# Performance work log

Measured on AMD Instinct MI355X. Metric: run time of the kernel, lower is better.

## Reference

```python
import jax, jax.numpy as jnp
import numpy as np

N = 100000
E = 1000000
HID = 64


def gcn_conv(x, W, b, edge_index, edge_w, num_nodes):
    # PyG GCNConv with edge_weight: add self-loops (weight 1), symmetric norm,
    # out[c] = sum_e norm_e * (x @ W)[row_e] aggregated at col_e, plus bias.
    xw = x @ W  # [N, hid]
    row = jnp.concatenate([edge_index[0], jnp.arange(num_nodes)])
    col = jnp.concatenate([edge_index[1], jnp.arange(num_nodes)])
    ew = jnp.concatenate([edge_w, jnp.ones((num_nodes,), x.dtype)])
    deg = jax.ops.segment_sum(ew, col, num_segments=num_nodes)
    dinv = jnp.where(deg > 0, jax.lax.rsqrt(deg), 0.0)
    norm = dinv[row] * ew * dinv[col]  # [E+N]
    msgs = norm[:, None] * xw[row]  # [E+N, hid]
    out = jax.ops.segment_sum(msgs, col, num_segments=num_nodes)
    return out + b


def setup_inputs() -> dict:
    key = jax.random.key(0)
    ks = jax.random.split(key, 12)
    user_x = jax.random.normal(ks[0], (N, 3), jnp.float32)
    movie_x = jax.random.normal(ks[1], (N, 18), jnp.float32)
    edge_index = jax.random.randint(ks[2], (2, E), 0, N, jnp.int64)
    edge_attr = jax.random.uniform(ks[3], (E,), jnp.float32)
    def lin(k, fan_in, fan_out):
        bound = 1.0 / np.sqrt(fan_in)
        k1, k2 = jax.random.split(k)
        W = jax.random.uniform(k1, (fan_in, fan_out), jnp.float32, -bound, bound)
        b = jax.random.uniform(k2, (fan_out,), jnp.float32, -bound, bound)
        return W, b
    W_user, b_user = lin(ks[4], 3, HID)
    W_movie, b_movie = lin(ks[5], 18, HID)
    W1, b1 = lin(ks[6], 2 * HID, 128)
    W2, b2 = lin(ks[7], 128, 1)
    return {"user_x": user_x, "movie_x": movie_x, "edge_index": edge_index,
            "edge_attr": edge_attr, "W_user": W_user, "b_user": b_user,
            "W_movie": W_movie, "b_movie": b_movie, "W1": W1, "b1": b1,
            "W2": W2, "b2": b2}


def reference(user_x, movie_x, edge_index, edge_attr, W_user, b_user,
              W_movie, b_movie, W1, b1, W2, b2):
    user_out = gcn_conv(user_x, W_user, b_user, edge_index, edge_attr, N)
    movie_out = gcn_conv(movie_x, W_movie, b_movie, edge_index, edge_attr, N)
    h = jnp.concatenate([user_out, movie_out], axis=-1)  # [N, 128]
    h = jax.nn.relu(h @ W1 + b1)
    rating_pred = h @ W2 + b2  # [N, 1]
    return rating_pred
```

## Files before the change

### kernel.cpp

```cpp
#include <hip/hip_runtime.h>

#define NN 100000
#define NE 1000000
#define BSH 7
#define BCOLS 128
#define NBUCK 782
#define SBLK 256
#define CAP 2048

__global__ __launch_bounds__(128) void fuse_kernel(const float* __restrict__ Wu,
                                                   const float* __restrict__ bu,
                                                   const float* __restrict__ Wm,
                                                   const float* __restrict__ bm,
                                                   const float* __restrict__ W1,
                                                   const float* __restrict__ b1,
                                                   const float* __restrict__ W2,
                                                   float* __restrict__ Mt,
                                                   int* __restrict__ cnt) {
    const int j = threadIdx.x;
    for (int i = j; i < NBUCK; i += 128) cnt[i] = 0;

    float w1c[128];
#pragma unroll
    for (int k = 0; k < 128; k++) w1c[k] = W1[k * 128 + j];

    float* row = Mt + j * 24;
#pragma unroll
    for (int m = 0; m < 3; m++) {
        float acc = 0.f;
#pragma unroll
        for (int k = 0; k < 64; k++) acc = fmaf(Wu[m * 64 + k], w1c[k], acc);
        row[m] = acc;
    }
#pragma unroll
    for (int m = 0; m < 18; m++) {
        float acc = 0.f;
#pragma unroll
        for (int k = 0; k < 64; k++) acc = fmaf(Wm[m * 64 + k], w1c[64 + k], acc);
        row[3 + m] = acc;
    }
    float bp = b1[j];
#pragma unroll
    for (int k = 0; k < 64; k++) {
        bp = fmaf(bu[k], w1c[k], bp);
        bp = fmaf(bm[k], w1c[64 + k], bp);
    }
    row[21] = bp;
    row[22] = W2[j];
    row[23] = 0.f;
}

__global__ __launch_bounds__(256) void bcnt_kernel(const int* __restrict__ col,
                                                   int* __restrict__ cnt) {
    __shared__ int h[NBUCK];
    for (int i = threadIdx.x; i < NBUCK; i += 256) h[i] = 0;
    __syncthreads();
    for (int e = blockIdx.x * 256 + threadIdx.x; e < NE; e += SBLK * 256)
        atomicAdd(&h[col[e] >> BSH], 1);
    __syncthreads();
    for (int i = threadIdx.x; i < NBUCK; i += 256)
        if (h[i]) atomicAdd(&cnt[i], h[i]);
}

__global__ __launch_bounds__(1024) void bscan_kernel(const int* __restrict__ cnt,
                                                     int* __restrict__ gbase,
                                                     int* __restrict__ H0) {
    __shared__ int s[1024];
    const int t = threadIdx.x;
    const int v = (t < NBUCK) ? cnt[t] : 0;
    s[t] = v;
    __syncthreads();
    for (int off = 1; off < 1024; off <<= 1) {
        int x = (t >= off) ? s[t - off] : 0;
        __syncthreads();
        s[t] += x;
        __syncthreads();
    }
    const int excl = s[t] - v;
    if (t < NBUCK) { gbase[t] = excl; H0[t] = excl; }
    if (t == 0) H0[NBUCK] = NE;
}

__global__ __launch_bounds__(256) void bscatter_kernel(const int* __restrict__ ei,
                                                       const float* __restrict__ ew,
                                                       int* __restrict__ gbase,
                                                       int2* __restrict__ mid) {
    __shared__ int h[NBUCK];
    __shared__ int rbase[NBUCK];
    for (int i = threadIdx.x; i < NBUCK; i += 256) h[i] = 0;
    __syncthreads();
    for (int e = blockIdx.x * 256 + threadIdx.x; e < NE; e += SBLK * 256)
        atomicAdd(&h[ei[NE + e] >> BSH], 1);
    __syncthreads();
    for (int i = threadIdx.x; i < NBUCK; i += 256) {
        const int c0 = h[i];
        rbase[i] = c0 ? atomicAdd(&gbase[i], c0) : 0;
        h[i] = 0;
    }
    __syncthreads();
    for (int e = blockIdx.x * 256 + threadIdx.x; e < NE; e += SBLK * 256) {
        const int c = ei[NE + e];
        const int r = ei[e];
        const float w = ew[e];
        const int b = c >> BSH;
        const int pos = rbase[b] + atomicAdd(&h[b], 1);
        mid[pos] = make_int2((c & (BCOLS - 1)) | (r << BSH), __float_as_int(w));
    }
}

__global__ __launch_bounds__(256) void bdeg_pack_kernel(const int2* __restrict__ mid,
                                                        const int* __restrict__ H0,
                                                        const float* __restrict__ ux,
                                                        const float* __restrict__ mx,
                                                        float* __restrict__ pack) {
    __shared__ float dl[BCOLS];
    const int b = blockIdx.x;
    const int t = threadIdx.x;
    if (t < BCOLS) dl[t] = 0.f;
    __syncthreads();
    const int start = H0[b];
    const int end = H0[b + 1];
    for (int i = start + t; i < end; i += 256) {
        const int2 p = mid[i];
        atomicAdd(&dl[p.x & (BCOLS - 1)], __int_as_float(p.y));
    }
    __syncthreads();
    if (t < BCOLS) {
        const int c = b * BCOLS + t;
        if (c < NN) dl[t] = rsqrtf(dl[t] + 1.0f);
    }
    __syncthreads();
    const size_t obase = (size_t)b * BCOLS * 24;
    for (int f = t; f < BCOLS * 24; f += 256) {
        const int rl = f / 24;
        const int m = f - rl * 24;
        const int r = b * BCOLS + rl;
        if (r < NN) {
            const float d = dl[rl];
            float v;
            if (m < 3) v = d * ux[(size_t)r * 3 + m];
            else if (m < 21) v = d * mx[(size_t)r * 18 + (m - 3)];
            else if (m == 21) v = d;
            else v = 0.f;
            pack[obase + f] = v;
        }
    }
}

__global__ __launch_bounds__(256) void bagg_mlp_kernel(const int2* __restrict__ mid,
                                                       const int* __restrict__ H0,
                                                       const float* __restrict__ pack,
                                                       const float* __restrict__ Mt,
                                                       const float* __restrict__ b2,
                                                       float* __restrict__ out) {
    __shared__ int2 smid[CAP];
    __shared__ int cbase[BCOLS];
    __shared__ int ccur[BCOLS];
    __shared__ float sp[BCOLS][21];
    __shared__ float po[BCOLS];

    const int b = blockIdx.x;
    const int t = threadIdx.x;
    const int col = t & (BCOLS - 1);
    const int hf = t >> 7;
    const int start = H0[b];
    const int end = H0[b + 1];
    const int seg = end - start;
    const int segc = seg < CAP ? seg : CAP;

    if (t < BCOLS) ccur[t] = 0;
    __syncthreads();
    for (int i = t; i < segc; i += 256)
        atomicAdd(&ccur[mid[start + i].x & (BCOLS - 1)], 1);
    __syncthreads();

    int myc = 0;
    if (t < BCOLS) { myc = ccur[t]; cbase[t] = myc; }
    __syncthreads();
    for (int off = 1; off < BCOLS; off <<= 1) {
        int x = 0;
        if (t < BCOLS && t >= off) x = cbase[t - off];
        __syncthreads();
        if (t < BCOLS) cbase[t] += x;
        __syncthreads();
    }
    if (t < BCOLS) ccur[t] = cbase[t] - myc;
    __syncthreads();

    for (int i = t; i < segc; i += 256) {
        const int2 p = mid[start + i];
        const int pos = atomicAdd(&ccur[p.x & (BCOLS - 1)], 1);
        smid[pos] = p;
    }
    __syncthreads();

    float s21[21];
#pragma unroll
    for (int m = 0; m < 21; m++) s21[m] = 0.f;

    const int s0 = (col == 0) ? 0 : cbase[col - 1];
    const int s1 = cbase[col];
#pragma unroll 2
    for (int i = s0 + hf; i < s1; i += 2) {
        const int2 p = smid[i];
        const unsigned row = ((unsigned)p.x) >> BSH;
        const float w = __int_as_float(p.y);
        const float4* pr = (const float4*)(pack + (size_t)row * 24);
        const float4 v0 = pr[0];
        const float4 v1 = pr[1];
        const float4 v2 = pr[2];
        const float4 v3 = pr[3];
        const float4 v4 = pr[4];
        const float4 v5 = pr[5];
        s21[0]  = fmaf(w, v0.x, s21[0]);
        s21[1]  = fmaf(w, v0.y, s21[1]);
        s21[2]  = fmaf(w, v0.z, s21[2]);
        s21[3]  = fmaf(w, v0.w, s21[3]);
        s21[4]  = fmaf(w, v1.x, s21[4]);
        s21[5]  = fmaf(w, v1.y, s21[5]);
        s21[6]  = fmaf(w, v1.z, s21[6]);
        s21[7]  = fmaf(w, v1.w, s21[7]);
        s21[8]  = fmaf(w, v2.x, s21[8]);
        s21[9]  = fmaf(w, v2.y, s21[9]);
        s21[10] = fmaf(w, v2.z, s21[10]);
        s21[11] = fmaf(w, v2.w, s21[11]);
        s21[12] = fmaf(w, v3.x, s21[12]);
        s21[13] = fmaf(w, v3.y, s21[13]);
        s21[14] = fmaf(w, v3.z, s21[14]);
        s21[15] = fmaf(w, v3.w, s21[15]);
        s21[16] = fmaf(w, v4.x, s21[16]);
        s21[17] = fmaf(w, v4.y, s21[17]);
        s21[18] = fmaf(w, v4.z, s21[18]);
        s21[19] = fmaf(w, v4.w, s21[19]);
        s21[20] = fmaf(w, v5.x, s21[20]);
    }

    if (hf) {
#pragma unroll
        for (int m = 0; m < 21; m++) sp[col][m] = s21[m];
    }
    __syncthreads();

    const int c = b * BCOLS + col;
    if (!hf) {
#pragma unroll
        for (int m = 0; m < 21; m++) s21[m] += sp[col][m];
        if (seg > CAP) {
            for (int i = CAP; i < seg; i++) {
                const int2 p = mid[start + i];
                if ((p.x & (BCOLS - 1)) == col) {
                    const unsigned row = ((unsigned)p.x) >> BSH;
                    const float w = __int_as_float(p.y);
                    const float* pr = pack + (size_t)row * 24;
#pragma unroll
                    for (int m = 0; m < 21; m++) s21[m] = fmaf(w, pr[m], s21[m]);
                }
            }
        }
        if (c < NN) {
            const float4* pr = (const float4*)(pack + (size_t)c * 24);
            const float4 v0 = pr[0];
            const float4 v1 = pr[1];
            const float4 v2 = pr[2];
            const float4 v3 = pr[3];
            const float4 v4 = pr[4];
            const float4 v5 = pr[5];
            const float d = v5.y;
            s21[0]  = d * (s21[0]  + v0.x);
            s21[1]  = d * (s21[1]  + v0.y);
            s21[2]  = d * (s21[2]  + v0.z);
            s21[3]  = d * (s21[3]  + v0.w);
            s21[4]  = d * (s21[4]  + v1.x);
            s21[5]  = d * (s21[5]  + v1.y);
            s21[6]  = d * (s21[6]  + v1.z);
            s21[7]  = d * (s21[7]  + v1.w);
            s21[8]  = d * (s21[8]  + v2.x);
            s21[9]  = d * (s21[9]  + v2.y);
            s21[10] = d * (s21[10] + v2.z);
            s21[11] = d * (s21[11] + v2.w);
            s21[12] = d * (s21[12] + v3.x);
            s21[13] = d * (s21[13] + v3.y);
            s21[14] = d * (s21[14] + v3.z);
            s21[15] = d * (s21[15] + v3.w);
            s21[16] = d * (s21[16] + v4.x);
            s21[17] = d * (s21[17] + v4.y);
            s21[18] = d * (s21[18] + v4.z);
            s21[19] = d * (s21[19] + v4.w);
            s21[20] = d * (s21[20] + v5.x);
        }
#pragma unroll
        for (int m = 0; m < 21; m++) sp[col][m] = s21[m];
    }
    __syncthreads();
    if (hf) {
#pragma unroll
        for (int m = 0; m < 21; m++) s21[m] = sp[col][m];
    }

    float o = 0.f;
    const int k0 = hf * 64;
#pragma unroll 4
    for (int k = k0; k < k0 + 64; k++) {
        const float* r = Mt + k * 24;
        float hsum = r[21];
#pragma unroll
        for (int m = 0; m < 21; m++) hsum = fmaf(s21[m], r[m], hsum);
        o = fmaf(fmaxf(hsum, 0.f), r[22], o);
    }
    if (hf) po[col] = o;
    __syncthreads();
    if (!hf && c < NN) out[c] = o + po[col] + b2[0];
}

extern "C" void kernel_launch(void* const* d_in, const int* in_sizes, int n_in,
                              void* d_out, int out_size, void* d_ws, size_t ws_size,
                              hipStream_t stream) {
    const float* ux = (const float*)d_in[0];
    const float* mx = (const float*)d_in[1];
    const int* ei = (const int*)d_in[2];
    const float* ew = (const float*)d_in[3];
    const float* Wu = (const float*)d_in[4];
    const float* bu = (const float*)d_in[5];
    const float* Wm = (const float*)d_in[6];
    const float* bm = (const float*)d_in[7];
    const float* W1 = (const float*)d_in[8];
    const float* b1 = (const float*)d_in[9];
    const float* W2 = (const float*)d_in[10];
    const float* b2 = (const float*)d_in[11];
    float* out = (float*)d_out;

    char* ws = (char*)d_ws;
    int*   cnt   = (int*)ws;
    int*   gbase = (int*)(ws + 4096);
    int*   H0    = (int*)(ws + 8192);
    float* Mt    = (float*)(ws + 12288);
    float* pack  = (float*)(ws + 24576);
    int2*  mid   = (int2*)(ws + 9624576);

    fuse_kernel<<<1, 128, 0, stream>>>(Wu, bu, Wm, bm, W1, b1, W2, Mt, cnt);
    bcnt_kernel<<<SBLK, 256, 0, stream>>>(ei + NE, cnt);
    bscan_kernel<<<1, 1024, 0, stream>>>(cnt, gbase, H0);
    bscatter_kernel<<<SBLK, 256, 0, stream>>>(ei, ew, gbase, mid);
    bdeg_pack_kernel<<<NBUCK, 256, 0, stream>>>(mid, H0, ux, mx, pack);
    bagg_mlp_kernel<<<NBUCK, 256, 0, stream>>>(mid, H0, pack, Mt, b2, out);
}
```

Measured before the change: 211.9 us.

## Store gathered node features in fp16 and restructure aggregation with wave shuffles

Node feature pack is stored as half2 (64B per row instead of 96B), with dinv in a separate fp32 array, to cut gather bandwidth in the aggregation kernel. The scatter kernel caches edge data in registers across the count and scatter passes instead of reloading. The aggregation kernel pairs adjacent threads per column and combines partials with shuffles rather than shared-memory syncs, and uses a wave-shuffle scan for the column offsets. fp16 storage loses precision in the aggregated features.

```diff
diff --git a/kernel.cpp b/kernel.cpp
--- a/kernel.cpp
+++ b/kernel.cpp
@@ -1,4 +1,5 @@
 #include <hip/hip_runtime.h>
+#include <hip/hip_fp16.h>
 
 #define NN 100000
 #define NE 1000000
@@ -6,7 +7,17 @@
 #define BCOLS 128
 #define NBUCK 782
 #define SBLK 256
+#define SITER 16
 #define CAP 2048
+
+__device__ __forceinline__ float2 h2f(unsigned u) {
+    union { unsigned u; __half2 h; } c; c.u = u;
+    return __half22float2(c.h);
+}
+__device__ __forceinline__ unsigned f2h2(float a, float b) {
+    union { __half2 h; unsigned u; } c; c.h = __floats2half2_rn(a, b);
+    return c.u;
+}
 
 __global__ __launch_bounds__(128) void fuse_kernel(const float* __restrict__ Wu,
                                                    const float* __restrict__ bu,
@@ -87,10 +98,22 @@
                                                        int2* __restrict__ mid) {
     __shared__ int h[NBUCK];
     __shared__ int rbase[NBUCK];
+    int cs[SITER], rs[SITER];
+    float wv[SITER];
+    const int e0 = blockIdx.x * 256 + threadIdx.x;
+
     for (int i = threadIdx.x; i < NBUCK; i += 256) h[i] = 0;
     __syncthreads();
-    for (int e = blockIdx.x * 256 + threadIdx.x; e < NE; e += SBLK * 256)
-        atomicAdd(&h[ei[NE + e] >> BSH], 1);
+#pragma unroll
+    for (int k = 0; k < SITER; k++) {
+        const int e = e0 + k * (SBLK * 256);
+        if (e < NE) {
+            cs[k] = ei[NE + e];
+            rs[k] = ei[e];
+            wv[k] = ew[e];
+            atomicAdd(&h[cs[k] >> BSH], 1);
+        }
+    }
     __syncthreads();
     for (int i = threadIdx.x; i < NBUCK; i += 256) {
         const int c0 = h[i];
@@ -98,13 +121,15 @@
         h[i] = 0;
     }
     __syncthreads();
-    for (int e = blockIdx.x * 256 + threadIdx.x; e < NE; e += SBLK * 256) {
-        const int c = ei[NE + e];
-        const int r = ei[e];
-        const float w = ew[e];
-        const int b = c >> BSH;
-        const int pos = rbase[b] + atomicAdd(&h[b], 1);
-        mid[pos] = make_int2((c & (BCOLS - 1)) | (r << BSH), __float_as_int(w));
+#pragma unroll
+    for (int k = 0; k < SITER; k++) {
+        const int e = e0 + k * (SBLK * 256);
+        if (e < NE) {
+            const int bb = cs[k] >> BSH;
+            const int pos = rbase[bb] + atomicAdd(&h[bb], 1);
+            mid[pos] = make_int2((cs[k] & (BCOLS - 1)) | (rs[k] << BSH),
+                                 __float_as_int(wv[k]));
+        }
     }
 }
 
@@ -112,7 +137,8 @@
                                                         const int* __restrict__ H0,
                                                         const float* __restrict__ ux,
                                                         const float* __restrict__ mx,
-                                                        float* __restrict__ pack) {
+                                                        unsigned short* __restrict__ pack16,
+                                                        float* __restrict__ dinv) {
     __shared__ float dl[BCOLS];
     const int b = blockIdx.x;
     const int t = threadIdx.x;
@@ -126,70 +152,100 @@
     }
     __syncthreads();
     if (t < BCOLS) {
-        const int c = b * BCOLS + t;
-        if (c < NN) dl[t] = rsqrtf(dl[t] + 1.0f);
-    }
-    __syncthreads();
-    const size_t obase = (size_t)b * BCOLS * 24;
-    for (int f = t; f < BCOLS * 24; f += 256) {
-        const int rl = f / 24;
-        const int m = f - rl * 24;
-        const int r = b * BCOLS + rl;
+        const int r = b * BCOLS + t;
         if (r < NN) {
-            const float d = dl[rl];
-            float v;
-            if (m < 3) v = d * ux[(size_t)r * 3 + m];
-            else if (m < 21) v = d * mx[(size_t)r * 18 + (m - 3)];
-            else if (m == 21) v = d;
-            else v = 0.f;
-            pack[obase + f] = v;
-        }
-    }
-}
+            const float d = rsqrtf(dl[t] + 1.0f);
+            dinv[r] = d;
+            float v[22];
+            const float* u = ux + (size_t)r * 3;
+            const float* m = mx + (size_t)r * 18;
+            v[0] = d * u[0];
+            v[1] = d * u[1];
+            v[2] = d * u[2];
+#pragma unroll
+            for (int k = 0; k < 18; k++) v[3 + k] = d * m[k];
+            v[21] = d;
+            unsigned wb[16];
+#pragma unroll
+            for (int k = 0; k < 11; k++) wb[k] = f2h2(v[2 * k], v[2 * k + 1]);
+#pragma unroll
+            for (int k = 11; k < 16; k++) wb[k] = 0u;
+            uint4* dst = (uint4*)(pack16 + (size_t)r * 32);
+            dst[0] = make_uint4(wb[0], wb[1], wb[2], wb[3]);
+            dst[1] = make_uint4(wb[4], wb[5], wb[6], wb[7]);
+            dst[2] = make_uint4(wb[8], wb[9], wb[10], wb[11]);
+            dst[3] = make_uint4(wb[12], wb[13], wb[14], wb[15]);
+        }
+    }
+}
+
+#define ACC_ROW(base)                                                        \
+    {                                                                        \
+        const uint4* pr_ = (const uint4*)(base);                             \
+        const uint4 A_ = pr_[0];                                             \
+        const uint4 B_ = pr_[1];                                             \
+        const uint2 C_ = ((const uint2*)pr_)[4];                             \
+        const unsigned D_ = ((const unsigned*)pr_)[10];                      \
+        float2 f_;                                                           \
+        f_ = h2f(A_.x); s21[0]  = fmaf(w, f_.x, s21[0]);  s21[1]  = fmaf(w, f_.y, s21[1]);  \
+        f_ = h2f(A_.y); s21[2]  = fmaf(w, f_.x, s21[2]);  s21[3]  = fmaf(w, f_.y, s21[3]);  \
+        f_ = h2f(A_.z); s21[4]  = fmaf(w, f_.x, s21[4]);  s21[5]  = fmaf(w, f_.y, s21[5]);  \
+        f_ = h2f(A_.w); s21[6]  = fmaf(w, f_.x, s21[6]);  s21[7]  = fmaf(w, f_.y, s21[7]);  \
+        f_ = h2f(B_.x); s21[8]  = fmaf(w, f_.x, s21[8]);  s21[9]  = fmaf(w, f_.y, s21[9]);  \
+        f_ = h2f(B_.y); s21[10] = fmaf(w, f_.x, s21[10]); s21[11] = fmaf(w, f_.y, s21[11]); \
+        f_ = h2f(B_.z); s21[12] = fmaf(w, f_.x, s21[12]); s21[13] = fmaf(w, f_.y, s21[13]); \
+        f_ = h2f(B_.w); s21[14] = fmaf(w, f_.x, s21[14]); s21[15] = fmaf(w, f_.y, s21[15]); \
+        f_ = h2f(C_.x); s21[16] = fmaf(w, f_.x, s21[16]); s21[17] = fmaf(w, f_.y, s21[17]); \
+        f_ = h2f(C_.y); s21[18] = fmaf(w, f_.x, s21[18]); s21[19] = fmaf(w, f_.y, s21[19]); \
+        f_ = h2f(D_);   s21[20] = fmaf(w, f_.x, s21[20]);                    \
+    }
 
 __global__ __launch_bounds__(256) void bagg_mlp_kernel(const int2* __restrict__ mid,
                                                        const int* __restrict__ H0,
-                                                       const float* __restrict__ pack,
+                                                       const unsigned short* __restrict__ pack16,
+                                                       const float* __restrict__ dinv,
                                                        const float* __restrict__ Mt,
                                                        const float* __restrict__ b2,
                                                        float* __restrict__ out) {
     __shared__ int2 smid[CAP];
+    __shared__ int ccnt[BCOLS];
     __shared__ int cbase[BCOLS];
-    __shared__ int ccur[BCOLS];
-    __shared__ float sp[BCOLS][21];
-    __shared__ float po[BCOLS];
+    __shared__ int cptr[BCOLS];
 
     const int b = blockIdx.x;
     const int t = threadIdx.x;
-    const int col = t & (BCOLS - 1);
-    const int hf = t >> 7;
+    const int col = t >> 1;
+    const int hf = t & 1;
     const int start = H0[b];
     const int end = H0[b + 1];
     const int seg = end - start;
     const int segc = seg < CAP ? seg : CAP;
 
-    if (t < BCOLS) ccur[t] = 0;
+    if (t < BCOLS) ccnt[t] = 0;
     __syncthreads();
     for (int i = t; i < segc; i += 256)
-        atomicAdd(&ccur[mid[start + i].x & (BCOLS - 1)], 1);
-    __syncthreads();
-
-    int myc = 0;
-    if (t < BCOLS) { myc = ccur[t]; cbase[t] = myc; }
-    __syncthreads();
-    for (int off = 1; off < BCOLS; off <<= 1) {
-        int x = 0;
-        if (t < BCOLS && t >= off) x = cbase[t - off];
-        __syncthreads();
-        if (t < BCOLS) cbase[t] += x;
-        __syncthreads();
-    }
-    if (t < BCOLS) ccur[t] = cbase[t] - myc;
+        atomicAdd(&ccnt[mid[start + i].x & (BCOLS - 1)], 1);
+    __syncthreads();
+
+    if (t < 64) {
+        const int a = ccnt[2 * t];
+        const int bb = ccnt[2 * t + 1];
+        int p = a + bb;
+#pragma unroll
+        for (int d = 1; d < 64; d <<= 1) {
+            const int x = __shfl_up(p, d, 64);
+            if (t >= d) p += x;
+        }
+        cbase[2 * t] = p - bb;
+        cbase[2 * t + 1] = p;
+        cptr[2 * t] = p - bb - a;
+        cptr[2 * t + 1] = p - bb;
+    }
     __syncthreads();
 
     for (int i = t; i < segc; i += 256) {
         const int2 p = mid[start + i];
-        const int pos = atomicAdd(&ccur[p.x & (BCOLS - 1)], 1);
+        const int pos = atomicAdd(&cptr[p.x & (BCOLS - 1)], 1);
         smid[pos] = p;
     }
     __syncthreads();
@@ -200,116 +256,51 @@
 
     const int s0 = (col == 0) ? 0 : cbase[col - 1];
     const int s1 = cbase[col];
-#pragma unroll 2
     for (int i = s0 + hf; i < s1; i += 2) {
         const int2 p = smid[i];
         const unsigned row = ((unsigned)p.x) >> BSH;
         const float w = __int_as_float(p.y);
-        const float4* pr = (const float4*)(pack + (size_t)row * 24);
-        const float4 v0 = pr[0];
-        const float4 v1 = pr[1];
-        const float4 v2 = pr[2];
-        const float4 v3 = pr[3];
-        const float4 v4 = pr[4];
-        const float4 v5 = pr[5];
-        s21[0]  = fmaf(w, v0.x, s21[0]);
-        s21[1]  = fmaf(w, v0.y, s21[1]);
-        s21[2]  = fmaf(w, v0.z, s21[2]);
-        s21[3]  = fmaf(w, v0.w, s21[3]);
-        s21[4]  = fmaf(w, v1.x, s21[4]);
-        s21[5]  = fmaf(w, v1.y, s21[5]);
-        s21[6]  = fmaf(w, v1.z, s21[6]);
-        s21[7]  = fmaf(w, v1.w, s21[7]);
-        s21[8]  = fmaf(w, v2.x, s21[8]);
-        s21[9]  = fmaf(w, v2.y, s21[9]);
-        s21[10] = fmaf(w, v2.z, s21[10]);
-        s21[11] = fmaf(w, v2.w, s21[11]);
-        s21[12] = fmaf(w, v3.x, s21[12]);
-        s21[13] = fmaf(w, v3.y, s21[13]);
-        s21[14] = fmaf(w, v3.z, s21[14]);
-        s21[15] = fmaf(w, v3.w, s21[15]);
-        s21[16] = fmaf(w, v4.x, s21[16]);
-        s21[17] = fmaf(w, v4.y, s21[17]);
-        s21[18] = fmaf(w, v4.z, s21[18]);
-        s21[19] = fmaf(w, v4.w, s21[19]);
-        s21[20] = fmaf(w, v5.x, s21[20]);
-    }
-
-    if (hf) {
-#pragma unroll
-        for (int m = 0; m < 21; m++) sp[col][m] = s21[m];
-    }
-    __syncthreads();
+        ACC_ROW(pack16 + (size_t)row * 32);
+    }
+    if (seg > CAP) {
+        for (int i = CAP + hf; i < seg; i += 2) {
+            const int2 p = mid[start + i];
+            if ((p.x & (BCOLS - 1)) == col) {
+                const unsigned row = ((unsigned)p.x) >> BSH;
+                const float w = __int_as_float(p.y);
+                ACC_ROW(pack16 + (size_t)row * 32);
+            }
+        }
+    }
+
+#pragma unroll
+    for (int m = 0; m < 21; m++) s21[m] += __shfl_xor(s21[m], 1, 64);
 
     const int c = b * BCOLS + col;
-    if (!hf) {
-#pragma unroll
-        for (int m = 0; m < 21; m++) s21[m] += sp[col][m];
-        if (seg > CAP) {
-            for (int i = CAP; i < seg; i++) {
-                const int2 p = mid[start + i];
-                if ((p.x & (BCOLS - 1)) == col) {
-                    const unsigned row = ((unsigned)p.x) >> BSH;
-                    const float w = __int_as_float(p.y);
-                    const float* pr = pack + (size_t)row * 24;
-#pragma unroll
-                    for (int m = 0; m < 21; m++) s21[m] = fmaf(w, pr[m], s21[m]);
-                }
-            }
-        }
-        if (c < NN) {
-            const float4* pr = (const float4*)(pack + (size_t)c * 24);
-            const float4 v0 = pr[0];
-            const float4 v1 = pr[1];
-            const float4 v2 = pr[2];
-            const float4 v3 = pr[3];
-            const float4 v4 = pr[4];
-            const float4 v5 = pr[5];
-            const float d = v5.y;
-            s21[0]  = d * (s21[0]  + v0.x);
-            s21[1]  = d * (s21[1]  + v0.y);
-            s21[2]  = d * (s21[2]  + v0.z);
-            s21[3]  = d * (s21[3]  + v0.w);
-            s21[4]  = d * (s21[4]  + v1.x);
-            s21[5]  = d * (s21[5]  + v1.y);
-            s21[6]  = d * (s21[6]  + v1.z);
-            s21[7]  = d * (s21[7]  + v1.w);
-            s21[8]  = d * (s21[8]  + v2.x);
-            s21[9]  = d * (s21[9]  + v2.y);
-            s21[10] = d * (s21[10] + v2.z);
-            s21[11] = d * (s21[11] + v2.w);
-            s21[12] = d * (s21[12] + v3.x);
-            s21[13] = d * (s21[13] + v3.y);
-            s21[14] = d * (s21[14] + v3.z);
-            s21[15] = d * (s21[15] + v3.w);
-            s21[16] = d * (s21[16] + v4.x);
-            s21[17] = d * (s21[17] + v4.y);
-            s21[18] = d * (s21[18] + v4.z);
-            s21[19] = d * (s21[19] + v4.w);
-            s21[20] = d * (s21[20] + v5.x);
-        }
-#pragma unroll
-        for (int m = 0; m < 21; m++) sp[col][m] = s21[m];
-    }
-    __syncthreads();
-    if (hf) {
-#pragma unroll
-        for (int m = 0; m < 21; m++) s21[m] = sp[col][m];
-    }
-
     float o = 0.f;
-    const int k0 = hf * 64;
+    if (c < NN) {
+        const float d = dinv[c];
+        {
+            const float w = 1.0f;
+            float* s21_alias = s21;
+            (void)s21_alias;
+            ACC_ROW(pack16 + (size_t)c * 32);
+        }
+#pragma unroll
+        for (int m = 0; m < 21; m++) s21[m] *= d;
+
+        const int k0 = hf * 64;
 #pragma unroll 4
-    for (int k = k0; k < k0 + 64; k++) {
-        const float* r = Mt + k * 24;
-        float hsum = r[21];
-#pragma unroll
-        for (int m = 0; m < 21; m++) hsum = fmaf(s21[m], r[m], hsum);
-        o = fmaf(fmaxf(hsum, 0.f), r[22], o);
-    }
-    if (hf) po[col] = o;
-    __syncthreads();
-    if (!hf && c < NN) out[c] = o + po[col] + b2[0];
+        for (int k = k0; k < k0 + 64; k++) {
+            const float* r = Mt + k * 24;
+            float hsum = r[21];
+#pragma unroll
+            for (int m = 0; m < 21; m++) hsum = fmaf(s21[m], r[m], hsum);
+            o = fmaf(fmaxf(hsum, 0.f), r[22], o);
+        }
+    }
+    o += __shfl_xor(o, 1, 64);
+    if (!hf && c < NN) out[c] = o + b2[0];
 }
 
 extern "C" void kernel_launch(void* const* d_in, const int* in_sizes, int n_in,
@@ -330,17 +321,18 @@
     float* out = (float*)d_out;
 
     char* ws = (char*)d_ws;
-    int*   cnt   = (int*)ws;
-    int*   gbase = (int*)(ws + 4096);
-    int*   H0    = (int*)(ws + 8192);
-    float* Mt    = (float*)(ws + 12288);
-    float* pack  = (float*)(ws + 24576);
-    int2*  mid   = (int2*)(ws + 9624576);
+    int*            cnt    = (int*)ws;
+    int*            gbase  = (int*)(ws + 4096);
+    int*            H0     = (int*)(ws + 8192);
+    float*          Mt     = (float*)(ws + 12288);
+    float*          dinv   = (float*)(ws + 24576);
+    unsigned short* pack16 = (unsigned short*)(ws + 424576);
+    int2*           mid    = (int2*)(ws + 6824576);
 
     fuse_kernel<<<1, 128, 0, stream>>>(Wu, bu, Wm, bm, W1, b1, W2, Mt, cnt);
     bcnt_kernel<<<SBLK, 256, 0, stream>>>(ei + NE, cnt);
     bscan_kernel<<<1, 1024, 0, stream>>>(cnt, gbase, H0);
     bscatter_kernel<<<SBLK, 256, 0, stream>>>(ei, ew, gbase, mid);
-    bdeg_pack_kernel<<<NBUCK, 256, 0, stream>>>(mid, H0, ux, mx, pack);
-    bagg_mlp_kernel<<<NBUCK, 256, 0, stream>>>(mid, H0, pack, Mt, b2, out);
-}
+    bdeg_pack_kernel<<<NBUCK, 256, 0, stream>>>(mid, H0, ux, mx, pack16, dinv);
+    bagg_mlp_kernel<<<NBUCK, 256, 0, stream>>>(mid, H0, pack16, dinv, Mt, b2, out);
+}
```

Result: slower. 245.1 us (+15.7%).
